# Kernel tuning notes

Hardware: AMD Instinct MI355X
Metric: run time of the kernel (lower is better)

Reference implementation:

```python
import jax, jax.numpy as jnp
import numpy as np

B, IN_DIM, UNITS = 16384, 3072, 3072  # batch, input_dim=3*unit1, units=3*unit2


def setup_inputs() -> dict:
    key = jax.random.key(0)
    k1, k2, k3 = jax.random.split(key, 3)
    inputs = jax.random.normal(k1, (B, IN_DIM), dtype=jnp.float32)
    # original init: uniform [0, 0.01) for w, zeros for b (gpe_bias = [0, 0])
    w = jax.random.uniform(k2, (IN_DIM, UNITS), dtype=jnp.float32, minval=0.0, maxval=0.01)
    b = jnp.zeros((UNITS,), dtype=jnp.float32)
    # per-unit binary diagonal mask, stored as [units, input_dim]
    mask = jax.random.randint(k3, (UNITS, IN_DIM), 0, 2, dtype=jnp.int32)
    return {"inputs": inputs, "w": w, "b": b, "mask": mask}


def reference(inputs, w, b, mask):
    # Original: p = transpose(s @ inputs^T, [2,0,1]) -> [batch, units, input_dim]
    #           f = diag_part(p @ w) + b            -> [batch, units]
    # Since s[u] = diag(mask[u]), this is exactly:
    #   f[b,u] = sum_i inputs[b,i] * mask[u,i] * w[i,u] + b[u]
    # i.e. a single masked GEMM with effective weight w * mask^T.
    w_eff = w * mask.T.astype(w.dtype)  # [input_dim, units]
    return inputs @ w_eff + b
```

## Files before the change

kernel.cpp:

```cpp
#include <hip/hip_runtime.h>

#define BATCH 16384
#define KDIM  3072
#define NDIM  3072

typedef __bf16 bf16;
typedef bf16  bf16x8  __attribute__((ext_vector_type(8)));
typedef float f32x16  __attribute__((ext_vector_type(16)));

__device__ __forceinline__ void g2l16(const bf16* g, bf16* l) {
    __builtin_amdgcn_global_load_lds(
        (__attribute__((address_space(1))) unsigned int*)g,
        (__attribute__((address_space(3))) unsigned int*)l,
        16, 0, 0);
}

__global__ __launch_bounds__(256) void cvt_a_kernel(const float* __restrict__ in,
                                                    bf16* __restrict__ out) {
    const long idx = (long)blockIdx.x * 256 + threadIdx.x;
    const float4* in4 = (const float4*)in;
    float4 a = in4[idx * 2];
    float4 b = in4[idx * 2 + 1];
    bf16x8 o;
    o[0] = (bf16)a.x; o[1] = (bf16)a.y; o[2] = (bf16)a.z; o[3] = (bf16)a.w;
    o[4] = (bf16)b.x; o[5] = (bf16)b.y; o[6] = (bf16)b.z; o[7] = (bf16)b.w;
    ((bf16x8*)out)[idx] = o;
}

__global__ __launch_bounds__(256) void weff_kernel(const float* __restrict__ w,
                                                   const int* __restrict__ mask,
                                                   bf16* __restrict__ wt) {
    __shared__ float tile[32][33];
    const int i0 = blockIdx.x * 32;
    const int u0 = blockIdx.y * 32;
    const int tx = threadIdx.x, ty = threadIdx.y;
#pragma unroll
    for (int r = 0; r < 4; r++)
        tile[ty + 8 * r][tx] = w[(long)(i0 + ty + 8 * r) * NDIM + u0 + tx];
    __syncthreads();
#pragma unroll
    for (int r = 0; r < 4; r++) {
        int u = u0 + ty + 8 * r;
        int i = i0 + tx;
        float v = tile[tx][ty + 8 * r] * (float)mask[(long)u * KDIM + i];
        wt[(long)u * KDIM + i] = (bf16)v;
    }
}

__global__ __launch_bounds__(256) void gemm_kernel(const bf16* __restrict__ A,
                                                   const bf16* __restrict__ Bt,
                                                   const float* __restrict__ bias,
                                                   float* __restrict__ C) {
    __shared__ __align__(16) bf16 lds[8192];

    const int tid  = threadIdx.x;
    const int lane = tid & 63;
    const int wv   = tid >> 6;
    const long m0 = (long)blockIdx.y * 128;
    const long n0 = (long)blockIdx.x * 128;
    const int waveM = (wv >> 1) * 64;
    const int waveN = (wv & 1) * 64;

    const int srow   = tid >> 2;
    const int schunk = (tid & 3) ^ ((tid >> 3) & 3);
    const bf16* gA = A + (m0 + srow) * KDIM + schunk * 8;
    const bf16* gB = Bt + (n0 + srow) * KDIM + schunk * 8;
    bf16* lA = &lds[tid * 8];
    bf16* lB = &lds[4096 + tid * 8];

    const int rl  = lane & 31;
    const int kb  = lane >> 5;
    const int rsw = (rl >> 1) & 3;
    const bf16* fA0 = &lds[(waveM + rl) * 32];
    const bf16* fB0 = &lds[4096 + (waveN + rl) * 32];
    const int c0 = ((0 + kb) ^ rsw) * 8;
    const int c1 = ((2 + kb) ^ rsw) * 8;

    f32x16 acc[2][2] = {};

    for (int k0 = 0; k0 < KDIM; k0 += 32) {
        __syncthreads();
        g2l16(gA, lA);
        g2l16(gA + 64 * KDIM, lA + 2048);
        g2l16(gB, lB);
        g2l16(gB + 64 * KDIM, lB + 2048);
        gA += 32;
        gB += 32;
        __syncthreads();

        bf16x8 a0[2], a1[2], b0[2], b1[2];
#pragma unroll
        for (int mi = 0; mi < 2; mi++) {
            a0[mi] = *(const bf16x8*)(fA0 + mi * 1024 + c0);
            a1[mi] = *(const bf16x8*)(fA0 + mi * 1024 + c1);
        }
#pragma unroll
        for (int ni = 0; ni < 2; ni++) {
            b0[ni] = *(const bf16x8*)(fB0 + ni * 1024 + c0);
            b1[ni] = *(const bf16x8*)(fB0 + ni * 1024 + c1);
        }
#pragma unroll
        for (int mi = 0; mi < 2; mi++)
#pragma unroll
            for (int ni = 0; ni < 2; ni++) {
                acc[mi][ni] = __builtin_amdgcn_mfma_f32_32x32x16_bf16(
                    a0[mi], b0[ni], acc[mi][ni], 0, 0, 0);
                acc[mi][ni] = __builtin_amdgcn_mfma_f32_32x32x16_bf16(
                    a1[mi], b1[ni], acc[mi][ni], 0, 0, 0);
            }
    }

#pragma unroll
    for (int mi = 0; mi < 2; mi++) {
#pragma unroll
        for (int ni = 0; ni < 2; ni++) {
            const long col  = n0 + waveN + ni * 32 + rl;
            const long rbase = m0 + waveM + mi * 32 + 4 * kb;
            const float bv = bias[col];
#pragma unroll
            for (int g = 0; g < 4; g++)
#pragma unroll
                for (int t = 0; t < 4; t++)
                    C[(rbase + 8 * g + t) * NDIM + col] = acc[mi][ni][4 * g + t] + bv;
        }
    }
}

__global__ __launch_bounds__(256) void naive_kernel(const float* __restrict__ x,
                                                    const float* __restrict__ w,
                                                    const float* __restrict__ bias,
                                                    const int* __restrict__ mask,
                                                    float* __restrict__ out) {
    const long idx = (long)blockIdx.x * 256 + threadIdx.x;
    const long bi = idx / NDIM;
    const int u = (int)(idx % NDIM);
    float s = 0.f;
    for (int k = 0; k < KDIM; k++)
        s += x[bi * KDIM + k] * w[(long)k * NDIM + u] * (float)mask[(long)u * KDIM + k];
    out[idx] = s + bias[u];
}

extern "C" void kernel_launch(void* const* d_in, const int* in_sizes, int n_in,
                              void* d_out, int out_size, void* d_ws, size_t ws_size,
                              hipStream_t stream) {
    const float* x    = (const float*)d_in[0];
    const float* w    = (const float*)d_in[1];
    const float* bias = (const float*)d_in[2];
    const int*   mask = (const int*)d_in[3];
    float* out = (float*)d_out;

    const size_t needA = (size_t)BATCH * KDIM * sizeof(bf16);
    const size_t needW = (size_t)NDIM * KDIM * sizeof(bf16);

    if (ws_size < needA + needW) {
        const long total = (long)BATCH * NDIM;
        naive_kernel<<<(int)(total / 256), 256, 0, stream>>>(x, w, bias, mask, out);
        return;
    }

    bf16* Abf = (bf16*)d_ws;
    bf16* Wt  = (bf16*)((char*)d_ws + needA);

    cvt_a_kernel<<<(BATCH * (KDIM / 8)) / 256, 256, 0, stream>>>(x, Abf);
    weff_kernel<<<dim3(KDIM / 32, NDIM / 32), dim3(32, 8), 0, stream>>>(w, mask, Wt);
    gemm_kernel<<<dim3(NDIM / 128, BATCH / 128), 256, 0, stream>>>(Abf, Wt, bias, out);
}
```

Measured before the change: 733.8 us.

## Double-buffer LDS and enlarge GEMM tile to 256x128 per block

The GEMM block tile grows from 128x128 to 256x128, with each wave computing a 128x64 sub-tile (4x2 MFMA accumulators). LDS is double-buffered so the next K-slice is prefetched via global_load_lds while the current one is computed, cutting one barrier per iteration. The XOR swizzle on LDS chunks is dropped, which may bring back LDS bank conflicts on fragment reads. More accumulators raise register pressure, and launch_bounds now requests 2 blocks per CU.

```diff
diff --git a/kernel.cpp b/kernel.cpp
--- a/kernel.cpp
+++ b/kernel.cpp
@@ -47,74 +47,77 @@
     }
 }
 
-__global__ __launch_bounds__(256) void gemm_kernel(const bf16* __restrict__ A,
-                                                   const bf16* __restrict__ Bt,
-                                                   const float* __restrict__ bias,
-                                                   float* __restrict__ C) {
-    __shared__ __align__(16) bf16 lds[8192];
+__global__ __launch_bounds__(256, 2) void gemm_kernel(const bf16* __restrict__ A,
+                                                      const bf16* __restrict__ Bt,
+                                                      const float* __restrict__ bias,
+                                                      float* __restrict__ C) {
+    __shared__ __align__(16) bf16 lds[2 * 12288];
 
     const int tid  = threadIdx.x;
     const int lane = tid & 63;
     const int wv   = tid >> 6;
-    const long m0 = (long)blockIdx.y * 128;
+    const long m0 = (long)blockIdx.y * 256;
     const long n0 = (long)blockIdx.x * 128;
-    const int waveM = (wv >> 1) * 64;
+    const int waveM = (wv >> 1) * 128;
     const int waveN = (wv & 1) * 64;
 
     const int srow   = tid >> 2;
-    const int schunk = (tid & 3) ^ ((tid >> 3) & 3);
+    const int schunk = tid & 3;
     const bf16* gA = A + (m0 + srow) * KDIM + schunk * 8;
     const bf16* gB = Bt + (n0 + srow) * KDIM + schunk * 8;
-    bf16* lA = &lds[tid * 8];
-    bf16* lB = &lds[4096 + tid * 8];
 
-    const int rl  = lane & 31;
-    const int kb  = lane >> 5;
-    const int rsw = (rl >> 1) & 3;
-    const bf16* fA0 = &lds[(waveM + rl) * 32];
-    const bf16* fB0 = &lds[4096 + (waveN + rl) * 32];
-    const int c0 = ((0 + kb) ^ rsw) * 8;
-    const int c1 = ((2 + kb) ^ rsw) * 8;
+    const int rl = lane & 31;
+    const int kb = lane >> 5;
+    const int aBase = (waveM + rl) * 32 + kb * 8;
+    const int bBase = 8192 + (waveN + rl) * 32 + kb * 8;
 
-    f32x16 acc[2][2] = {};
+    f32x16 acc[4][2] = {};
 
-    for (int k0 = 0; k0 < KDIM; k0 += 32) {
+    {
+        bf16* d = &lds[tid * 8];
+#pragma unroll
+        for (int j = 0; j < 4; j++) g2l16(gA + (long)(64 * j) * KDIM, d + j * 2048);
+#pragma unroll
+        for (int j = 0; j < 2; j++) g2l16(gB + (long)(64 * j) * KDIM, d + 8192 + j * 2048);
+    }
+    __syncthreads();
+
+    for (int i = 0; i < KDIM / 32; ++i) {
+        const int p = i & 1;
+        if (i + 1 < KDIM / 32) {
+            const long ko = (long)(i + 1) * 32;
+            bf16* d = &lds[(1 - p) * 12288 + tid * 8];
+#pragma unroll
+            for (int j = 0; j < 4; j++) g2l16(gA + (long)(64 * j) * KDIM + ko, d + j * 2048);
+#pragma unroll
+            for (int j = 0; j < 2; j++) g2l16(gB + (long)(64 * j) * KDIM + ko, d + 8192 + j * 2048);
+        }
+
+        const bf16* bp = &lds[p * 12288];
+#pragma unroll
+        for (int t = 0; t < 2; t++) {
+            bf16x8 a[4], b[2];
+#pragma unroll
+            for (int mi = 0; mi < 4; mi++)
+                a[mi] = *(const bf16x8*)(bp + aBase + mi * 1024 + t * 16);
+#pragma unroll
+            for (int ni = 0; ni < 2; ni++)
+                b[ni] = *(const bf16x8*)(bp + bBase + ni * 1024 + t * 16);
+#pragma unroll
+            for (int mi = 0; mi < 4; mi++)
+#pragma unroll
+                for (int ni = 0; ni < 2; ni++)
+                    acc[mi][ni] = __builtin_amdgcn_mfma_f32_32x32x16_bf16(
+                        a[mi], b[ni], acc[mi][ni], 0, 0, 0);
+        }
         __syncthreads();
-        g2l16(gA, lA);
-        g2l16(gA + 64 * KDIM, lA + 2048);
-        g2l16(gB, lB);
-        g2l16(gB + 64 * KDIM, lB + 2048);
-        gA += 32;
-        gB += 32;
-        __syncthreads();
-
-        bf16x8 a0[2], a1[2], b0[2], b1[2];
-#pragma unroll
-        for (int mi = 0; mi < 2; mi++) {
-            a0[mi] = *(const bf16x8*)(fA0 + mi * 1024 + c0);
-            a1[mi] = *(const bf16x8*)(fA0 + mi * 1024 + c1);
-        }
-#pragma unroll
-        for (int ni = 0; ni < 2; ni++) {
-            b0[ni] = *(const bf16x8*)(fB0 + ni * 1024 + c0);
-            b1[ni] = *(const bf16x8*)(fB0 + ni * 1024 + c1);
-        }
-#pragma unroll
-        for (int mi = 0; mi < 2; mi++)
-#pragma unroll
-            for (int ni = 0; ni < 2; ni++) {
-                acc[mi][ni] = __builtin_amdgcn_mfma_f32_32x32x16_bf16(
-                    a0[mi], b0[ni], acc[mi][ni], 0, 0, 0);
-                acc[mi][ni] = __builtin_amdgcn_mfma_f32_32x32x16_bf16(
-                    a1[mi], b1[ni], acc[mi][ni], 0, 0, 0);
-            }
     }
 
 #pragma unroll
-    for (int mi = 0; mi < 2; mi++) {
+    for (int mi = 0; mi < 4; mi++) {
 #pragma unroll
         for (int ni = 0; ni < 2; ni++) {
-            const long col  = n0 + waveN + ni * 32 + rl;
+            const long col   = n0 + waveN + ni * 32 + rl;
             const long rbase = m0 + waveM + mi * 32 + 4 * kb;
             const float bv = bias[col];
 #pragma unroll
@@ -163,5 +166,5 @@
 
     cvt_a_kernel<<<(BATCH * (KDIM / 8)) / 256, 256, 0, stream>>>(x, Abf);
     weff_kernel<<<dim3(KDIM / 32, NDIM / 32), dim3(32, 8), 0, stream>>>(w, mask, Wt);
-    gemm_kernel<<<dim3(NDIM / 128, BATCH / 128), 256, 0, stream>>>(Abf, Wt, bias, out);
+    gemm_kernel<<<dim3(NDIM / 128, BATCH / 256), 256, 0, stream>>>(Abf, Wt, bias, out);
 }
```

New measurement: 691.3 us. -5.8%, faster.
